# Kernel optimization log

Measured on AMD Instinct MI355X. Metric: run time of the kernel, lower is better.

## Reference

```python
import jax, jax.numpy as jnp
import numpy as np

EPS = 1e-6


def _rmsnorm(x, w, eps=EPS):
    # x: (..., d); normalize over last dim
    ms = jnp.mean(jnp.square(x), axis=-1, keepdims=True)
    return x * jax.lax.rsqrt(ms + eps) * w


def setup_inputs() -> dict:
    key = jax.random.key(0)
    ks = jax.random.split(key, 5)
    B, S, D = 2, 2048, 2048
    n_heads, n_kv = 16, 4
    d_head = D // n_heads  # 128
    sd = 1.0 / np.sqrt(D)
    return {
        "x": jax.random.normal(ks[0], (B, S, D), dtype=jnp.float32),
        "wq": jax.random.normal(ks[1], (D, n_heads * d_head), dtype=jnp.float32) * sd,
        "wk": jax.random.normal(ks[2], (D, n_kv * d_head), dtype=jnp.float32) * sd,
        "wv": jax.random.normal(ks[3], (D, n_kv * d_head), dtype=jnp.float32) * sd,
        "wo": jax.random.normal(ks[4], (D, D), dtype=jnp.float32) * sd,
        "q_norm_w": jnp.ones((d_head,), dtype=jnp.float32),
        "k_norm_w": jnp.ones((d_head,), dtype=jnp.float32),
    }


def reference(x, wq, wk, wv, wo, q_norm_w, k_norm_w):
    B, S, D = x.shape
    n_heads, n_kv = 16, 4
    groups = n_heads // n_kv
    d_head = D // n_heads

    # QKV projections (bias=False)
    q = (x @ wq).reshape(B, S, n_kv, groups, d_head)  # q heads grouped by kv head
    k = (x @ wk).reshape(B, S, n_kv, d_head)
    v = (x @ wv).reshape(B, S, n_kv, d_head)

    # qk RMSNorm over d_head
    q = _rmsnorm(q, q_norm_w)
    k = _rmsnorm(k, k_norm_w)

    # GQA attention without materializing expanded K/V:
    # scores: (B, n_kv, groups, S_q, S_k)
    scale = 1.0 / jnp.sqrt(jnp.asarray(d_head, dtype=x.dtype))
    scores = jnp.einsum('bskgd,btkd->bkgst', q, k) * scale
    causal = jnp.tril(jnp.ones((S, S), dtype=bool))
    scores = jnp.where(causal, scores, jnp.asarray(-jnp.inf, dtype=scores.dtype))
    attn = jax.nn.softmax(scores, axis=-1)
    out = jnp.einsum('bkgst,btkd->bskgd', attn, v)  # (B, S, n_kv, groups, d_head)
    out = out.reshape(B, S, D)
    return out @ wo
```

## Files before the change

kernel.cpp:

```cpp
#include <hip/hip_runtime.h>
#include <hip/hip_bf16.h>
#include <stdint.h>

typedef unsigned short u16;
typedef __attribute__((ext_vector_type(8))) short short8;
typedef __attribute__((ext_vector_type(4))) float f32x4;
typedef __attribute__((ext_vector_type(16))) float f32x16;

__device__ __forceinline__ u16 f2bf(float f){
  union { __hip_bfloat16 h; u16 u; } v; v.h = __float2bfloat16(f); return v.u;
}
__device__ __forceinline__ float bf2f(u16 h){
  union { uint32_t u; float f; } v; v.u = ((uint32_t)h) << 16;
  return v.f;
}
__device__ __forceinline__ f32x4 mfma16(short8 a, short8 b, f32x4 c){
  return __builtin_amdgcn_mfma_f32_16x16x32_bf16(a, b, c, 0, 0, 0);
}
__device__ __forceinline__ f32x16 mfma32(short8 a, short8 b, f32x16 c){
  return __builtin_amdgcn_mfma_f32_32x32x16_bf16(a, b, c, 0, 0, 0);
}
__device__ __forceinline__ void gl_lds16(const u16* g, u16* l){
  __builtin_amdgcn_global_load_lds((const __attribute__((address_space(1))) void*)g,
                                   (__attribute__((address_space(3))) void*)l, 16, 0, 0);
}
template<int N> __device__ __forceinline__ void waitvm(){
  if constexpr (N==0) asm volatile("s_waitcnt vmcnt(0)" ::: "memory");
  else if constexpr (N==2) asm volatile("s_waitcnt vmcnt(2)" ::: "memory");
  else if constexpr (N==4) asm volatile("s_waitcnt vmcnt(4)" ::: "memory");
  else if constexpr (N==8) asm volatile("s_waitcnt vmcnt(8)" ::: "memory");
  else static_assert(N==0 || N==2 || N==4 || N==8, "unsupported vmcnt");
}
__device__ __forceinline__ void phase_sep(){
  __builtin_amdgcn_sched_barrier(0);
  __builtin_amdgcn_s_barrier();
  __builtin_amdgcn_sched_barrier(0);
}
__device__ __forceinline__ uint32_t cvtpk(float lo, float hi){
  uint32_t r;
  asm("v_cvt_pk_bf16_f32 %0, %1, %2" : "=v"(r) : "v"(lo), "v"(hi));
  return r;
}

__global__ __launch_bounds__(256) void cvt_x(const float* __restrict__ s,
                                             u16* __restrict__ d, int n4){
  const int i = blockIdx.x*256 + threadIdx.x;
  if (i >= n4) return;
  const float4 v = ((const float4*)s)[i];
  ushort4 pk;
  pk.x = f2bf(v.x); pk.y = f2bf(v.y); pk.z = f2bf(v.z); pk.w = f2bf(v.w);
  ((ushort4*)d)[i] = pk;
}

__global__ __launch_bounds__(256) void transpose_cvt(const float* __restrict__ src,
    u16* __restrict__ dst, int R, int C)
{
  __shared__ float tile[32][33];
  const int tx = threadIdx.x, ty = threadIdx.y;
  const int c0 = blockIdx.x << 5, r0 = blockIdx.y << 5;
  #pragma unroll
  for (int i=0;i<4;i++)
    tile[ty + (i<<3)][tx] = src[(size_t)(r0 + ty + (i<<3))*C + c0 + tx];
  __syncthreads();
  #pragma unroll
  for (int i=0;i<4;i++)
    dst[(size_t)(c0 + ty + (i<<3))*R + r0 + tx] = f2bf(tile[tx][ty + (i<<3)]);
}

__global__ __launch_bounds__(256) void v_transpose(const u16* __restrict__ qkv,
    u16* __restrict__ vT)
{
  __shared__ u16 tile[32][33];
  const int tx = threadIdx.x, ty = threadIdx.y;
  const int s0 = blockIdx.x << 5, d0 = blockIdx.y << 5;
  const int bk = blockIdx.z; const int b = bk >> 2, kv = bk & 3;
  const u16* src = qkv + (size_t)b*2048*3072 + 2560 + kv*128;
  #pragma unroll
  for (int i=0;i<4;i++)
    tile[ty + (i<<3)][tx] = src[(size_t)(s0 + ty + (i<<3))*3072 + d0 + tx];
  __syncthreads();
  u16* dst = vT + (size_t)((b<<2)+kv)*128*2048;
  #pragma unroll
  for (int i=0;i<4;i++)
    dst[(size_t)(d0 + ty + (i<<3))*2048 + s0 + tx] = tile[tx][ty + (i<<3)];
}

__global__ __launch_bounds__(256) void rmsnorm_qk(u16* __restrict__ qkv,
    const float* __restrict__ qw, const float* __restrict__ kw)
{
  const int lane = threadIdx.x & 63;
  const int rid = blockIdx.x*4 + (threadIdx.x >> 6);
  const int row = rid / 20;
  const int slot = rid % 20;
  u16* p = qkv + (size_t)row*3072 + slot*128 + (lane<<1);
  const u16 r0 = p[0], r1 = p[1];
  const float a = bf2f(r0), c = bf2f(r1);
  float ss = a*a + c*c;
  #pragma unroll
  for (int off=1; off<64; off<<=1) ss += __shfl_xor(ss, off);
  float sc = rsqrtf(ss*(1.0f/128.0f) + 1e-6f);
  if (slot < 16) sc *= 0.1275187952317199f;
  const float* wp = (slot < 16) ? qw : kw;
  const float w0 = wp[lane<<1], w1 = wp[(lane<<1)+1];
  p[0] = f2bf(a*sc*w0);
  p[1] = f2bf(c*sc*w1);
}

template<int BM, int CBF16>
__global__ __launch_bounds__(512, 2) void gemm8(const u16* __restrict__ A,
    const u16* __restrict__ BT, void* __restrict__ Cp,
    int M, int N, int K, int ldc)
{
  constexpr int MF   = BM/32;
  constexpr int MQ   = MF/2;
  constexpr int AH   = BM/2;
  constexpr int ASZ  = AH*64;
  constexpr int DBUF = 2*ASZ + 16384;
  constexpr int WV   = (BM==256) ? 4 : 2;
  __shared__ u16 lds[2*DBUF];
  const int tid = threadIdx.x;
  const int w = tid >> 6, lane = tid & 63;
  const int l15 = lane & 15, lg = lane >> 4;
  const int wm = w >> 2, wn = w & 3;
  const int nbx = N >> 8;
  const int nwg = gridDim.x;
  int bid = blockIdx.x;
  bid = (bid & 7) * (nwg >> 3) + (bid >> 3);
  const int m0 = (bid / nbx) * BM;
  const int n0 = (bid % nbx) << 8;

  const u16* gA0 = A  + (size_t)m0*K;
  const u16* gA1 = gA0 + (size_t)AH*K;
  const u16* gB0 = BT + (size_t)n0*K;
  const u16* gB1 = gB0 + (size_t)128*K;

  auto slotA = [&](int d, int h)->u16*{ return lds + d*DBUF + h*ASZ; };
  auto slotB = [&](int d, int h)->u16*{ return lds + d*DBUF + 2*ASZ + h*8192; };

  auto stage_half = [&](const u16* gbase, int kt, u16* sbase, int rows){
    const int iters = rows >> 6;
    for (int i=0;i<iters;i++){
      const int p = (i<<9) + tid;
      const int row = p>>3, sg = (p&7) ^ (row&7);
      gl_lds16(gbase + (size_t)row*K + (kt<<6) + (sg<<3), sbase + (p<<3));
    }
  };
  auto stA = [&](int kt, int d){ stage_half(gA0, kt, slotA(d,0), AH);
                                 stage_half(gA1, kt, slotA(d,1), AH); };
  auto stB = [&](int kt, int d){ stage_half(gB0, kt, slotB(d,0), 128);
                                 stage_half(gB1, kt, slotB(d,1), 128); };
  auto frag_at = [&](const u16* buf, int lrow, int kk)->short8{
    const int s = ((kk<<2)+lg) ^ (lrow&7);
    return *(const short8*)(buf + (((lrow<<3)+s)<<3));
  };

  short8 af[MQ][2], bfe[2][2], bfo[2][2];
  f32x4 acc[MF][4];
  #pragma unroll
  for (int m=0;m<MF;m++)
    #pragma unroll
    for (int n=0;n<4;n++) acc[m][n] = (f32x4){0.f,0.f,0.f,0.f};

  const int bh = wn>>1;
  const int brow0 = ((wn&1)<<6) + l15;

  auto rd_a = [&](const u16* buf, int mq){
    #pragma unroll
    for (int m=0;m<MQ;m++)
      #pragma unroll
      for (int kk=0;kk<2;kk++)
        af[m][kk] = frag_at(buf, mq*(BM>>2) + (m<<4) + l15, kk);
  };
  auto rd_b = [&](const u16* buf, int nq, short8 (*dst)[2]){
    #pragma unroll
    for (int n=0;n<2;n++)
      #pragma unroll
      for (int kk=0;kk<2;kk++)
        dst[n][kk] = frag_at(buf, brow0 + (nq<<5) + (n<<4), kk);
  };
  auto do_mfma = [&](int mb, int nb, short8 (*bf)[2]){
    __builtin_amdgcn_s_setprio(1);
    #pragma unroll
    for (int m=0;m<MQ;m++)
      #pragma unroll
      for (int n=0;n<2;n++)
        #pragma unroll
        for (int kk=0;kk<2;kk++)
          acc[mb+m][nb+n] = mfma16(af[m][kk], bf[n][kk], acc[mb+m][nb+n]);
    __builtin_amdgcn_s_setprio(0);
  };

  stA(0,0); stB(0,0); stA(1,1);
  waitvm<WV>();
  phase_sep();

  const int niter = K >> 7;
  for (int i=0; i<niter; ++i){
    const bool full = (i+1 < niter);
    const int t1 = 2*i+1;
    rd_a(slotA(0,wm), 0); rd_b(slotB(0,bh), 0, bfe);
    stB(t1, 1);
    phase_sep();
    do_mfma(0, 0, bfe);
    phase_sep();
    rd_b(slotB(0,bh), 1, bfo);
    phase_sep();
    do_mfma(0, 2, bfo);
    phase_sep();
    rd_a(slotA(0,wm), 1);
    phase_sep();
    do_mfma(MQ, 2, bfo);
    phase_sep();
    rd_b(slotB(0,bh), 0, bfe);
    if (full) stA(t1+1, 0);
    phase_sep();
    do_mfma(MQ, 0, bfe);
    if (full) waitvm<WV>(); else waitvm<0>();
    phase_sep();
    rd_a(slotA(1,wm), 0); rd_b(slotB(1,bh), 0, bfe);
    if (full) stB(t1+1, 0);
    phase_sep();
    do_mfma(0, 0, bfe);
    phase_sep();
    rd_b(slotB(1,bh), 1, bfo);
    phase_sep();
    do_mfma(0, 2, bfo);
    phase_sep();
    rd_a(slotA(1,wm), 1);
    phase_sep();
    do_mfma(MQ, 2, bfo);
    phase_sep();
    rd_b(slotB(1,bh), 0, bfe);
    if (full) stA(t1+2, 1);
    phase_sep();
    do_mfma(MQ, 0, bfe);
    if (full) waitvm<WV>();
    phase_sep();
  }

  #pragma unroll
  for (int m=0;m<MF;m++){
    #pragma unroll
    for (int n=0;n<4;n++){
      const int col = n0 + (wn<<6) + (n<<4) + l15;
      #pragma unroll
      for (int r=0;r<4;r++){
        const int row = m0 + wm*AH + (m<<4) + (lg<<2) + r;
        if (CBF16) ((u16*)Cp)[(size_t)row*ldc + col] = f2bf(acc[m][n][r]);
        else       ((float*)Cp)[(size_t)row*ldc + col] = acc[m][n][r];
      }
    }
  }
}

__global__ __launch_bounds__(256, 2) void attn_kernel(const u16* __restrict__ qkv,
    const u16* __restrict__ vT, u16* __restrict__ aout)
{
  __shared__ u16 Klds[2][8192];
  __shared__ u16 Vlds[8192];
  const int tid = threadIdx.x;
  const int w = tid >> 6, lane = tid & 63;
  const int l31 = lane & 31, hi = lane >> 5;
  const int bx = blockIdx.x, h = blockIdx.y, b = blockIdx.z;
  const int qI = b ? bx : (15 - bx);
  const int kvh = h >> 2;
  const int qb = qI*128 + (w<<5);
  const int nt = 2*qI + 2;

  const u16* qkvb = qkv + (size_t)b*2048*3072;
  short8 qf[8];
  {
    const u16* qp = qkvb + (size_t)(qb + l31)*3072 + h*128 + hi*8;
    #pragma unroll
    for (int kk=0;kk<8;kk++) qf[kk] = *(const short8*)(qp + kk*16);
  }
  f32x16 oacc[4];
  #pragma unroll
  for (int d=0;d<4;d++)
    #pragma unroll
    for (int r=0;r<16;r++) oacc[d][r] = 0.f;
  float m_run = -__builtin_inff(), lsum = 0.f;

  const u16* kb_ = qkvb + 2048 + kvh*128;
  const u16* vb_ = vT + (size_t)((b<<2)+kvh)*128*2048;

  auto stageK = [&](int t, int buf){
    #pragma unroll
    for (int i=0;i<4;i++){
      const int u = (i<<8) + tid;
      const int row = u>>4, d0 = (u&15) ^ (row&15);
      gl_lds16(kb_ + (size_t)((t<<6)+row)*3072 + (d0<<3), &Klds[buf][u<<3]);
    }
  };
  auto stageV = [&](int t){
    #pragma unroll
    for (int i=0;i<4;i++){
      const int u = (i<<8) + tid;
      const int rp = u>>4, z = (u&15) ^ (rp&15);
      const int d = (rp<<1) + (z>>3), k8 = z&7;
      gl_lds16(vb_ + (size_t)d*2048 + (t<<6) + (k8<<3), &Vlds[u<<3]);
    }
  };

  stageK(0, 0);
  int kbuf = 0;
  for (int t=0; t<nt; ++t){
    const bool pre = (t+1 < nt);
    stageV(t);
    if (pre) stageK(t+1, kbuf^1);
    if (pre) waitvm<8>(); else waitvm<4>();
    phase_sep();
    const int t0 = t<<6;
    const bool act = (t0 <= qb + 31);
    uint32_t paw[4][4];
    if (act){
      f32x16 s0, s1;
      #pragma unroll
      for (int r=0;r<16;r++){ s0[r] = 0.f; s1[r] = 0.f; }
      #pragma unroll
      for (int kk=0;kk<8;kk++){
        const int d0 = (kk<<1) + hi;
        const short8 k0 = *(const short8*)&Klds[kbuf][((l31<<4) + (d0 ^ (l31&15)))<<3];
        s0 = mfma32(k0, qf[kk], s0);
        const int r1 = 32 + l31;
        const short8 k1 = *(const short8*)&Klds[kbuf][((r1<<4) + (d0 ^ (r1&15)))<<3];
        s1 = mfma32(k1, qf[kk], s1);
      }
      if (t0 + 63 > qb){
        const int qrel = qb + l31 - t0;
        #pragma unroll
        for (int r=0;r<16;r++){
          const int kloc = (r&3) + ((r>>2)<<3) + (hi<<2);
          if (kloc      > qrel) s0[r] = -__builtin_inff();
          if (kloc + 32 > qrel) s1[r] = -__builtin_inff();
        }
      }
      float t8[8];
      #pragma unroll
      for (int i=0;i<8;i++) t8[i] = fmaxf(fmaxf(s0[i], s0[i+8]), fmaxf(s1[i], s1[i+8]));
      #pragma unroll
      for (int i=0;i<4;i++) t8[i] = fmaxf(t8[i], t8[i+4]);
      float mx = fmaxf(fmaxf(t8[0],t8[1]), fmaxf(t8[2],t8[3]));
      mx = fmaxf(mx, __shfl_xor(mx, 32));
      const bool noskip = !__all(mx - m_run <= 8.0f);
      const float mnew = noskip ? fmaxf(m_run, mx) : m_run;
      float rs = 0.f;
      #pragma unroll
      for (int i=0;i<16;i++){
        s0[i] = __builtin_amdgcn_exp2f(s0[i] - mnew);
        s1[i] = __builtin_amdgcn_exp2f(s1[i] - mnew);
        rs += s0[i] + s1[i];
      }
      rs += __shfl_xor(rs, 32);
      if (noskip){
        const float corr = __builtin_amdgcn_exp2f(m_run - mnew);
        m_run = mnew;
        lsum = lsum*corr + rs;
        #pragma unroll
        for (int r=0;r<16;r++){
          const float cr = __shfl(corr, (r&3) + ((r>>2)<<3) + (hi<<2));
          #pragma unroll
          for (int db=0;db<4;db++) oacc[db][r] *= cr;
        }
      } else {
        lsum += rs;
      }
      #pragma unroll
      for (int kk=0;kk<4;kk++){
        const int base = (kk&1)<<3;
        float v0,v1,v2,v3,v4,v5,v6,v7;
        if (kk<2){ v0=s0[base+0]; v1=s0[base+1]; v2=s0[base+2]; v3=s0[base+3];
                   v4=s0[base+4]; v5=s0[base+5]; v6=s0[base+6]; v7=s0[base+7]; }
        else     { v0=s1[base+0]; v1=s1[base+1]; v2=s1[base+2]; v3=s1[base+3];
                   v4=s1[base+4]; v5=s1[base+5]; v6=s1[base+6]; v7=s1[base+7]; }
        uint32_t a0 = cvtpk(v0, v1), a1 = cvtpk(v2, v3);
        uint32_t b0 = cvtpk(v4, v5), b1 = cvtpk(v6, v7);
        asm volatile("v_permlane32_swap_b32 %0, %1" : "+v"(a0), "+v"(b0));
        asm volatile("v_permlane32_swap_b32 %0, %1" : "+v"(a1), "+v"(b1));
        paw[kk][0] = a0; paw[kk][1] = a1; paw[kk][2] = b0; paw[kk][3] = b1;
      }
    }
    if (pre) waitvm<4>(); else waitvm<0>();
    phase_sep();
    if (act){
      #pragma unroll
      for (int kk=0;kk<4;kk++){
        union { uint32_t w[4]; short8 v; } pu;
        pu.w[0]=paw[kk][0]; pu.w[1]=paw[kk][1]; pu.w[2]=paw[kk][2]; pu.w[3]=paw[kk][3];
        const short8 pa = pu.v;
        #pragma unroll
        for (int db=0;db<4;db++){
          const int d = (db<<5) + l31, rp = d>>1;
          const int sl = (((d&1)<<3) | ((kk<<1)+hi)) ^ (rp&15);
          const short8 vv = *(const short8*)&Vlds[((rp<<4)+sl)<<3];
          oacc[db] = mfma32(pa, vv, oacc[db]);
        }
      }
    }
    phase_sep();
    kbuf ^= 1;
  }

  const float inv = 1.0f / lsum;
  #pragma unroll
  for (int r=0;r<16;r++){
    const int qr = (r&3) + ((r>>2)<<3) + (hi<<2);
    const float ivr = __shfl(inv, qr);
    u16* op = aout + (size_t)(b*2048 + qb + qr)*2048 + h*128 + l31;
    #pragma unroll
    for (int db=0;db<4;db++)
      op[db<<5] = f2bf(oacc[db][r] * ivr);
  }
}

extern "C" void kernel_launch(void* const* d_in, const int* in_sizes, int n_in,
                              void* d_out, int out_size, void* d_ws, size_t ws_size,
                              hipStream_t stream) {
  const float* x  = (const float*)d_in[0];
  const float* wq = (const float*)d_in[1];
  const float* wk = (const float*)d_in[2];
  const float* wv = (const float*)d_in[3];
  const float* wo = (const float*)d_in[4];
  const float* qw = (const float*)d_in[5];
  const float* kw = (const float*)d_in[6];
  char* ws = (char*)d_ws;
  u16* xbf   = (u16*)(ws);
  u16* wqkvT = (u16*)(ws + 16777216);
  u16* woT   = (u16*)(ws + 29360128);
  u16* qkv   = (u16*)(ws + 37748736);
  u16* vT    = (u16*)(ws + 62914560);
  float* out = (float*)d_out;

  dim3 tb(32,8);
  cvt_x<<<8192, 256, 0, stream>>>(x, xbf, 2097152);
  transpose_cvt<<<dim3(64,64), tb, 0, stream>>>(wq, wqkvT,             2048, 2048);
  transpose_cvt<<<dim3(16,64), tb, 0, stream>>>(wk, wqkvT + 2048*2048, 2048, 512);
  transpose_cvt<<<dim3(16,64), tb, 0, stream>>>(wv, wqkvT + 2560*2048, 2048, 512);
  transpose_cvt<<<dim3(64,64), tb, 0, stream>>>(wo, woT,               2048, 2048);
  gemm8<256,1><<<192, 512, 0, stream>>>(xbf, wqkvT, qkv, 4096, 3072, 2048, 3072);
  rmsnorm_qk<<<20480, 256, 0, stream>>>(qkv, qw, kw);
  v_transpose<<<dim3(64,4,8), tb, 0, stream>>>(qkv, vT);
  attn_kernel<<<dim3(16,16,2), 256, 0, stream>>>(qkv, vT, xbf);
  gemm8<128,0><<<256, 512, 0, stream>>>(xbf, woT, out, 4096, 2048, 2048, 2048);
}
```

Baseline: 196.6 us.

## Split long causal attention rows across two blocks and merge with a combine kernel

Query blocks 8-15 now have their KV range split into two halves, each handled by a separate workgroup that writes unnormalized partial outputs plus running max and sum. A new combine kernel merges the two halves with log-sum-exp weights. A constant table orders the 768 work items longest-first for load balancing, and launch bounds go up to 3 blocks per CU. The aim is to fix the causal load imbalance and tail effect, at the cost of an extra kernel launch and fp32 partial traffic. The partials are staged in the output buffer and the weight workspace before those are overwritten.

```diff
diff --git a/kernel.cpp b/kernel.cpp
--- a/kernel.cpp
+++ b/kernel.cpp
@@ -6,6 +6,10 @@
 typedef __attribute__((ext_vector_type(8))) short short8;
 typedef __attribute__((ext_vector_type(4))) float f32x4;
 typedef __attribute__((ext_vector_type(16))) float f32x16;
+
+__constant__ unsigned char TJ[24] = {
+  39, 15, 31, 14, 30, 38, 13, 29, 12, 28, 37, 11,
+  27, 10, 26, 36,  9, 25,  8, 24, 35, 34, 33, 32 };
 
 __device__ __forceinline__ u16 f2bf(float f){
   union { __hip_bfloat16 h; u16 u; } v; v.h = __float2bfloat16(f); return v.u;
@@ -253,19 +257,25 @@
   }
 }
 
-__global__ __launch_bounds__(256, 2) void attn_kernel(const u16* __restrict__ qkv,
-    const u16* __restrict__ vT, u16* __restrict__ aout)
+__global__ __launch_bounds__(256, 3) void attn_kernel(const u16* __restrict__ qkv,
+    const u16* __restrict__ vT, u16* __restrict__ aout,
+    float* __restrict__ partial, float2* __restrict__ mlbuf)
 {
   __shared__ u16 Klds[2][8192];
   __shared__ u16 Vlds[8192];
   const int tid = threadIdx.x;
   const int w = tid >> 6, lane = tid & 63;
   const int l31 = lane & 31, hi = lane >> 5;
-  const int bx = blockIdx.x, h = blockIdx.y, b = blockIdx.z;
-  const int qI = b ? bx : (15 - bx);
-  const int kvh = h >> 2;
+  const int bid = blockIdx.x;
+  const int j = bid >> 5;
+  const int grp = bid & 31;
+  const int b = grp >> 4, kvh = (grp >> 2) & 3, hh = grp & 3;
+  const int h = (kvh<<2) + hh;
+  const unsigned v_ = TJ[j];
+  const int qI = v_ & 15, s = v_ >> 4;
+  const int tb = (s == 1) ? (qI + 1) : 0;
+  const int te = (s == 0) ? (qI + 1) : (2*qI + 2);
   const int qb = qI*128 + (w<<5);
-  const int nt = 2*qI + 2;
 
   const u16* qkvb = qkv + (size_t)b*2048*3072;
   short8 qf[8];
@@ -302,114 +312,152 @@
     }
   };
 
-  stageK(0, 0);
+  stageK(tb, 0);
   int kbuf = 0;
-  for (int t=0; t<nt; ++t){
-    const bool pre = (t+1 < nt);
+  for (int t=tb; t<te; ++t){
+    const bool pre = (t+1 < te);
     stageV(t);
     if (pre) stageK(t+1, kbuf^1);
     if (pre) waitvm<8>(); else waitvm<4>();
     phase_sep();
     const int t0 = t<<6;
-    const bool act = (t0 <= qb + 31);
+    f32x16 s0, s1;
+    #pragma unroll
+    for (int r=0;r<16;r++){ s0[r] = 0.f; s1[r] = 0.f; }
+    #pragma unroll
+    for (int kk=0;kk<8;kk++){
+      const int d0 = (kk<<1) + hi;
+      const short8 k0 = *(const short8*)&Klds[kbuf][((l31<<4) + (d0 ^ (l31&15)))<<3];
+      s0 = mfma32(k0, qf[kk], s0);
+      const int r1 = 32 + l31;
+      const short8 k1 = *(const short8*)&Klds[kbuf][((r1<<4) + (d0 ^ (r1&15)))<<3];
+      s1 = mfma32(k1, qf[kk], s1);
+    }
+    if (t0 + 63 > qb){
+      const int qrel = qb + l31 - t0;
+      #pragma unroll
+      for (int r=0;r<16;r++){
+        const int kloc = (r&3) + ((r>>2)<<3) + (hi<<2);
+        if (kloc      > qrel) s0[r] = -__builtin_inff();
+        if (kloc + 32 > qrel) s1[r] = -__builtin_inff();
+      }
+    }
+    float t8[8];
+    #pragma unroll
+    for (int i=0;i<8;i++) t8[i] = fmaxf(fmaxf(s0[i], s0[i+8]), fmaxf(s1[i], s1[i+8]));
+    #pragma unroll
+    for (int i=0;i<4;i++) t8[i] = fmaxf(t8[i], t8[i+4]);
+    float mx = fmaxf(fmaxf(t8[0],t8[1]), fmaxf(t8[2],t8[3]));
+    mx = fmaxf(mx, __shfl_xor(mx, 32));
+    const bool noskip = !__all(mx - m_run <= 8.0f);
+    const float mnew = noskip ? fmaxf(m_run, mx) : m_run;
+    float rs = 0.f;
+    #pragma unroll
+    for (int i=0;i<16;i++){
+      s0[i] = __builtin_amdgcn_exp2f(s0[i] - mnew);
+      s1[i] = __builtin_amdgcn_exp2f(s1[i] - mnew);
+      rs += s0[i] + s1[i];
+    }
+    rs += __shfl_xor(rs, 32);
+    if (noskip){
+      const float corr = __builtin_amdgcn_exp2f(m_run - mnew);
+      m_run = mnew;
+      lsum = lsum*corr + rs;
+      #pragma unroll
+      for (int r=0;r<16;r++){
+        const float cr = __shfl(corr, (r&3) + ((r>>2)<<3) + (hi<<2));
+        #pragma unroll
+        for (int db=0;db<4;db++) oacc[db][r] *= cr;
+      }
+    } else {
+      lsum += rs;
+    }
     uint32_t paw[4][4];
-    if (act){
-      f32x16 s0, s1;
-      #pragma unroll
-      for (int r=0;r<16;r++){ s0[r] = 0.f; s1[r] = 0.f; }
-      #pragma unroll
-      for (int kk=0;kk<8;kk++){
-        const int d0 = (kk<<1) + hi;
-        const short8 k0 = *(const short8*)&Klds[kbuf][((l31<<4) + (d0 ^ (l31&15)))<<3];
-        s0 = mfma32(k0, qf[kk], s0);
-        const int r1 = 32 + l31;
-        const short8 k1 = *(const short8*)&Klds[kbuf][((r1<<4) + (d0 ^ (r1&15)))<<3];
-        s1 = mfma32(k1, qf[kk], s1);
+    #pragma unroll
+    for (int kk=0;kk<4;kk++){
+      const int base = (kk&1)<<3;
+      float v0,v1,v2,v3,v4,v5,v6,v7;
+      if (kk<2){ v0=s0[base+0]; v1=s0[base+1]; v2=s0[base+2]; v3=s0[base+3];
+                 v4=s0[base+4]; v5=s0[base+5]; v6=s0[base+6]; v7=s0[base+7]; }
+      else     { v0=s1[base+0]; v1=s1[base+1]; v2=s1[base+2]; v3=s1[base+3];
+                 v4=s1[base+4]; v5=s1[base+5]; v6=s1[base+6]; v7=s1[base+7]; }
+      uint32_t a0 = cvtpk(v0, v1), a1 = cvtpk(v2, v3);
+      uint32_t b0 = cvtpk(v4, v5), b1 = cvtpk(v6, v7);
+      asm volatile("v_permlane32_swap_b32 %0, %1" : "+v"(a0), "+v"(b0));
+      asm volatile("v_permlane32_swap_b32 %0, %1" : "+v"(a1), "+v"(b1));
+      paw[kk][0] = a0; paw[kk][1] = a1; paw[kk][2] = b0; paw[kk][3] = b1;
+    }
+    if (pre) waitvm<4>(); else waitvm<0>();
+    phase_sep();
+    #pragma unroll
+    for (int kk=0;kk<4;kk++){
+      union { uint32_t w[4]; short8 v; } pu;
+      pu.w[0]=paw[kk][0]; pu.w[1]=paw[kk][1]; pu.w[2]=paw[kk][2]; pu.w[3]=paw[kk][3];
+      const short8 pa = pu.v;
+      #pragma unroll
+      for (int db=0;db<4;db++){
+        const int d = (db<<5) + l31, rp = d>>1;
+        const int sl = (((d&1)<<3) | ((kk<<1)+hi)) ^ (rp&15);
+        const short8 vv = *(const short8*)&Vlds[((rp<<4)+sl)<<3];
+        oacc[db] = mfma32(pa, vv, oacc[db]);
       }
-      if (t0 + 63 > qb){
-        const int qrel = qb + l31 - t0;
-        #pragma unroll
-        for (int r=0;r<16;r++){
-          const int kloc = (r&3) + ((r>>2)<<3) + (hi<<2);
-          if (kloc      > qrel) s0[r] = -__builtin_inff();
-          if (kloc + 32 > qrel) s1[r] = -__builtin_inff();
-        }
-      }
-      float t8[8];
-      #pragma unroll
-      for (int i=0;i<8;i++) t8[i] = fmaxf(fmaxf(s0[i], s0[i+8]), fmaxf(s1[i], s1[i+8]));
-      #pragma unroll
-      for (int i=0;i<4;i++) t8[i] = fmaxf(t8[i], t8[i+4]);
-      float mx = fmaxf(fmaxf(t8[0],t8[1]), fmaxf(t8[2],t8[3]));
-      mx = fmaxf(mx, __shfl_xor(mx, 32));
-      const bool noskip = !__all(mx - m_run <= 8.0f);
-      const float mnew = noskip ? fmaxf(m_run, mx) : m_run;
-      float rs = 0.f;
-      #pragma unroll
-      for (int i=0;i<16;i++){
-        s0[i] = __builtin_amdgcn_exp2f(s0[i] - mnew);
-        s1[i] = __builtin_amdgcn_exp2f(s1[i] - mnew);
-        rs += s0[i] + s1[i];
-      }
-      rs += __shfl_xor(rs, 32);
-      if (noskip){
-        const float corr = __builtin_amdgcn_exp2f(m_run - mnew);
-        m_run = mnew;
-        lsum = lsum*corr + rs;
-        #pragma unroll
-        for (int r=0;r<16;r++){
-          const float cr = __shfl(corr, (r&3) + ((r>>2)<<3) + (hi<<2));
-          #pragma unroll
-          for (int db=0;db<4;db++) oacc[db][r] *= cr;
-        }
-      } else {
-        lsum += rs;
-      }
-      #pragma unroll
-      for (int kk=0;kk<4;kk++){
-        const int base = (kk&1)<<3;
-        float v0,v1,v2,v3,v4,v5,v6,v7;
-        if (kk<2){ v0=s0[base+0]; v1=s0[base+1]; v2=s0[base+2]; v3=s0[base+3];
-                   v4=s0[base+4]; v5=s0[base+5]; v6=s0[base+6]; v7=s0[base+7]; }
-        else     { v0=s1[base+0]; v1=s1[base+1]; v2=s1[base+2]; v3=s1[base+3];
-                   v4=s1[base+4]; v5=s1[base+5]; v6=s1[base+6]; v7=s1[base+7]; }
-        uint32_t a0 = cvtpk(v0, v1), a1 = cvtpk(v2, v3);
-        uint32_t b0 = cvtpk(v4, v5), b1 = cvtpk(v6, v7);
-        asm volatile("v_permlane32_swap_b32 %0, %1" : "+v"(a0), "+v"(b0));
-        asm volatile("v_permlane32_swap_b32 %0, %1" : "+v"(a1), "+v"(b1));
-        paw[kk][0] = a0; paw[kk][1] = a1; paw[kk][2] = b0; paw[kk][3] = b1;
-      }
-    }
-    if (pre) waitvm<4>(); else waitvm<0>();
-    phase_sep();
-    if (act){
-      #pragma unroll
-      for (int kk=0;kk<4;kk++){
-        union { uint32_t w[4]; short8 v; } pu;
-        pu.w[0]=paw[kk][0]; pu.w[1]=paw[kk][1]; pu.w[2]=paw[kk][2]; pu.w[3]=paw[kk][3];
-        const short8 pa = pu.v;
-        #pragma unroll
-        for (int db=0;db<4;db++){
-          const int d = (db<<5) + l31, rp = d>>1;
-          const int sl = (((d&1)<<3) | ((kk<<1)+hi)) ^ (rp&15);
-          const short8 vv = *(const short8*)&Vlds[((rp<<4)+sl)<<3];
-          oacc[db] = mfma32(pa, vv, oacc[db]);
-        }
-      }
     }
     phase_sep();
     kbuf ^= 1;
   }
 
-  const float inv = 1.0f / lsum;
-  #pragma unroll
-  for (int r=0;r<16;r++){
-    const int qr = (r&3) + ((r>>2)<<3) + (hi<<2);
-    const float ivr = __shfl(inv, qr);
-    u16* op = aout + (size_t)(b*2048 + qb + qr)*2048 + h*128 + l31;
-    #pragma unroll
-    for (int db=0;db<4;db++)
-      op[db<<5] = f2bf(oacc[db][r] * ivr);
+  if (s == 2){
+    const float inv = 1.0f / lsum;
+    #pragma unroll
+    for (int r=0;r<16;r++){
+      const int qr = (r&3) + ((r>>2)<<3) + (hi<<2);
+      const float ivr = __shfl(inv, qr);
+      u16* op = aout + (size_t)(b*2048 + qI*128 + (w<<5) + qr)*2048 + h*128 + l31;
+      #pragma unroll
+      for (int db=0;db<4;db++)
+        op[db<<5] = f2bf(oacc[db][r] * ivr);
+    }
+  } else {
+    const int tau = (((b<<4) + h)<<3) + (qI - 8);
+    float* pO = partial + (size_t)((tau<<1)+s)*16384;
+    #pragma unroll
+    for (int r=0;r<16;r++){
+      const int qr = (r&3) + ((r>>2)<<3) + (hi<<2);
+      float* pr = pO + ((w<<5)+qr)*128 + l31;
+      #pragma unroll
+      for (int db=0;db<4;db++) pr[db<<5] = oacc[db][r];
+    }
+    if (hi == 0)
+      mlbuf[((tau<<1)+s)*128 + (w<<5) + l31] = make_float2(m_run, lsum);
+  }
+}
+
+__global__ __launch_bounds__(256) void attn_combine(const float* __restrict__ partial,
+    const float2* __restrict__ mlbuf, u16* __restrict__ aout)
+{
+  const int tau = blockIdx.x;
+  const int b = tau >> 7, h = (tau >> 3) & 15, qI = (tau & 7) + 8;
+  const int row = threadIdx.x >> 1;
+  const int c0 = (threadIdx.x & 1) << 6;
+  const float2 ml0 = mlbuf[(tau<<1)*128 + row];
+  const float2 ml1 = mlbuf[((tau<<1)+1)*128 + row];
+  const float M = fmaxf(ml0.x, ml1.x);
+  float w0 = __builtin_amdgcn_exp2f(ml0.x - M);
+  float w1 = __builtin_amdgcn_exp2f(ml1.x - M);
+  const float inv = 1.0f / (w0*ml0.y + w1*ml1.y);
+  w0 *= inv; w1 *= inv;
+  const float4* P0 = (const float4*)(partial + (size_t)(tau<<1)*16384 + row*128 + c0);
+  const float4* P1 = (const float4*)(partial + (size_t)((tau<<1)+1)*16384 + row*128 + c0);
+  ushort4* op = (ushort4*)(aout + (size_t)(b*2048 + qI*128 + row)*2048 + h*128 + c0);
+  #pragma unroll
+  for (int i=0;i<16;i++){
+    const float4 a = P0[i], c = P1[i];
+    ushort4 o;
+    o.x = f2bf(w0*a.x + w1*c.x);
+    o.y = f2bf(w0*a.y + w1*c.y);
+    o.z = f2bf(w0*a.z + w1*c.z);
+    o.w = f2bf(w0*a.w + w1*c.w);
+    op[i] = o;
   }
 }
 
@@ -429,6 +477,7 @@
   u16* woT   = (u16*)(ws + 29360128);
   u16* qkv   = (u16*)(ws + 37748736);
   u16* vT    = (u16*)(ws + 62914560);
+  float2* ml = (float2*)(ws + 16777216);
   float* out = (float*)d_out;
 
   dim3 tb(32,8);
@@ -440,6 +489,7 @@
   gemm8<256,1><<<192, 512, 0, stream>>>(xbf, wqkvT, qkv, 4096, 3072, 2048, 3072);
   rmsnorm_qk<<<20480, 256, 0, stream>>>(qkv, qw, kw);
   v_transpose<<<dim3(64,4,8), tb, 0, stream>>>(qkv, vT);
-  attn_kernel<<<dim3(16,16,2), 256, 0, stream>>>(qkv, vT, xbf);
+  attn_kernel<<<768, 256, 0, stream>>>(qkv, vT, xbf, out, ml);
+  attn_combine<<<256, 256, 0, stream>>>(out, ml, xbf);
   gemm8<128,0><<<256, 512, 0, stream>>>(xbf, woT, out, 4096, 2048, 2048, 2048);
 }
```

New measurement: 234.4 us. 1.19x slower.

## Pair high and low causal query tiles per block sharing K/V tiles

Applied to the files above, without the earlier changes.

Each attention block now handles two 128-row query tiles, one from the top and one from the bottom of the causal range, so every block does equal work and each K/V tile staged in LDS serves both. V is double-buffered alongside K, with loads issued two tiles ahead, and the grid is halved with launch bounds lowered to one block per SIMD slot. This aims to remove causal load imbalance and halve K/V traffic per query row. In exchange, register pressure roughly doubles (two accumulator sets), occupancy drops, and only 256 blocks are launched.

```diff
diff --git a/kernel.cpp b/kernel.cpp
--- a/kernel.cpp
+++ b/kernel.cpp
@@ -253,163 +253,189 @@
   }
 }
 
-__global__ __launch_bounds__(256, 2) void attn_kernel(const u16* __restrict__ qkv,
+__global__ __launch_bounds__(256, 1) void attn_kernel(const u16* __restrict__ qkv,
     const u16* __restrict__ vT, u16* __restrict__ aout)
 {
   __shared__ u16 Klds[2][8192];
-  __shared__ u16 Vlds[8192];
+  __shared__ u16 Vlds[2][8192];
   const int tid = threadIdx.x;
   const int w = tid >> 6, lane = tid & 63;
   const int l31 = lane & 31, hi = lane >> 5;
-  const int bx = blockIdx.x, h = blockIdx.y, b = blockIdx.z;
-  const int qI = b ? bx : (15 - bx);
+  const int h = blockIdx.x, p = blockIdx.y, b = blockIdx.z;
   const int kvh = h >> 2;
-  const int qb = qI*128 + (w<<5);
-  const int nt = 2*qI + 2;
+  const int hq0 = (15-p) << 7, lq0 = p << 7;
+  const int nt = 32 - 2*p;
+  const int qbH = hq0 + (w<<5), qbL = lq0 + (w<<5);
 
   const u16* qkvb = qkv + (size_t)b*2048*3072;
-  short8 qf[8];
+  short8 qfH[8], qfL[8];
   {
-    const u16* qp = qkvb + (size_t)(qb + l31)*3072 + h*128 + hi*8;
-    #pragma unroll
-    for (int kk=0;kk<8;kk++) qf[kk] = *(const short8*)(qp + kk*16);
+    const u16* qpH = qkvb + (size_t)(qbH + l31)*3072 + h*128 + hi*8;
+    const u16* qpL = qkvb + (size_t)(qbL + l31)*3072 + h*128 + hi*8;
+    #pragma unroll
+    for (int kk=0;kk<8;kk++){ qfH[kk] = *(const short8*)(qpH + kk*16);
+                              qfL[kk] = *(const short8*)(qpL + kk*16); }
   }
-  f32x16 oacc[4];
+  f32x16 oaccH[4], oaccL[4];
   #pragma unroll
   for (int d=0;d<4;d++)
     #pragma unroll
-    for (int r=0;r<16;r++) oacc[d][r] = 0.f;
-  float m_run = -__builtin_inff(), lsum = 0.f;
+    for (int r=0;r<16;r++){ oaccH[d][r] = 0.f; oaccL[d][r] = 0.f; }
+  float mH = -__builtin_inff(), lH = 0.f;
+  float mL = -__builtin_inff(), lL = 0.f;
 
   const u16* kb_ = qkvb + 2048 + kvh*128;
   const u16* vb_ = vT + (size_t)((b<<2)+kvh)*128*2048;
 
-  auto stageK = [&](int t, int buf){
+  auto stageKV = [&](int t, int buf){
     #pragma unroll
     for (int i=0;i<4;i++){
       const int u = (i<<8) + tid;
       const int row = u>>4, d0 = (u&15) ^ (row&15);
       gl_lds16(kb_ + (size_t)((t<<6)+row)*3072 + (d0<<3), &Klds[buf][u<<3]);
     }
-  };
-  auto stageV = [&](int t){
     #pragma unroll
     for (int i=0;i<4;i++){
       const int u = (i<<8) + tid;
       const int rp = u>>4, z = (u&15) ^ (rp&15);
       const int d = (rp<<1) + (z>>3), k8 = z&7;
-      gl_lds16(vb_ + (size_t)d*2048 + (t<<6) + (k8<<3), &Vlds[u<<3]);
-    }
-  };
-
-  stageK(0, 0);
-  int kbuf = 0;
+      gl_lds16(vb_ + (size_t)d*2048 + (t<<6) + (k8<<3), &Vlds[buf][u<<3]);
+    }
+  };
+
+  auto qksm = [&](const u16* Kb, const short8* qf, f32x16* oacc,
+                  float& m_run, float& lsum, int qb, int t0,
+                  uint32_t paw[4][4]){
+    f32x16 s0, s1;
+    #pragma unroll
+    for (int r=0;r<16;r++){ s0[r] = 0.f; s1[r] = 0.f; }
+    #pragma unroll
+    for (int kk=0;kk<8;kk++){
+      const int d0 = (kk<<1) + hi;
+      const short8 k0 = *(const short8*)&Kb[((l31<<4) + (d0 ^ (l31&15)))<<3];
+      s0 = mfma32(k0, qf[kk], s0);
+      const int r1 = 32 + l31;
+      const short8 k1 = *(const short8*)&Kb[((r1<<4) + (d0 ^ (r1&15)))<<3];
+      s1 = mfma32(k1, qf[kk], s1);
+    }
+    if (t0 + 63 > qb){
+      const int qrel = qb + l31 - t0;
+      #pragma unroll
+      for (int r=0;r<16;r++){
+        const int kloc = (r&3) + ((r>>2)<<3) + (hi<<2);
+        if (kloc      > qrel) s0[r] = -__builtin_inff();
+        if (kloc + 32 > qrel) s1[r] = -__builtin_inff();
+      }
+    }
+    float t8[8];
+    #pragma unroll
+    for (int i=0;i<8;i++) t8[i] = fmaxf(fmaxf(s0[i], s0[i+8]), fmaxf(s1[i], s1[i+8]));
+    #pragma unroll
+    for (int i=0;i<4;i++) t8[i] = fmaxf(t8[i], t8[i+4]);
+    float mx = fmaxf(fmaxf(t8[0],t8[1]), fmaxf(t8[2],t8[3]));
+    mx = fmaxf(mx, __shfl_xor(mx, 32));
+    const bool noskip = !__all(mx - m_run <= 8.0f);
+    const float mnew = noskip ? fmaxf(m_run, mx) : m_run;
+    float rs = 0.f;
+    #pragma unroll
+    for (int i=0;i<16;i++){
+      s0[i] = __builtin_amdgcn_exp2f(s0[i] - mnew);
+      s1[i] = __builtin_amdgcn_exp2f(s1[i] - mnew);
+      rs += s0[i] + s1[i];
+    }
+    rs += __shfl_xor(rs, 32);
+    if (noskip){
+      const float corr = __builtin_amdgcn_exp2f(m_run - mnew);
+      m_run = mnew;
+      lsum = lsum*corr + rs;
+      #pragma unroll
+      for (int r=0;r<16;r++){
+        const float cr = __shfl(corr, (r&3) + ((r>>2)<<3) + (hi<<2));
+        #pragma unroll
+        for (int db=0;db<4;db++) oacc[db][r] *= cr;
+      }
+    } else {
+      lsum += rs;
+    }
+    #pragma unroll
+    for (int kk=0;kk<4;kk++){
+      const int base = (kk&1)<<3;
+      float v0,v1,v2,v3,v4,v5,v6,v7;
+      if (kk<2){ v0=s0[base+0]; v1=s0[base+1]; v2=s0[base+2]; v3=s0[base+3];
+                 v4=s0[base+4]; v5=s0[base+5]; v6=s0[base+6]; v7=s0[base+7]; }
+      else     { v0=s1[base+0]; v1=s1[base+1]; v2=s1[base+2]; v3=s1[base+3];
+                 v4=s1[base+4]; v5=s1[base+5]; v6=s1[base+6]; v7=s1[base+7]; }
+      uint32_t a0 = cvtpk(v0, v1), a1 = cvtpk(v2, v3);
+      uint32_t b0 = cvtpk(v4, v5), b1 = cvtpk(v6, v7);
+      asm volatile("v_permlane32_swap_b32 %0, %1" : "+v"(a0), "+v"(b0));
+      asm volatile("v_permlane32_swap_b32 %0, %1" : "+v"(a1), "+v"(b1));
+      paw[kk][0] = a0; paw[kk][1] = a1; paw[kk][2] = b0; paw[kk][3] = b1;
+    }
+  };
+
+  auto mkpa = [&](const uint32_t pw[4])->short8{
+    union { uint32_t w[4]; short8 v; } pu;
+    pu.w[0]=pw[0]; pu.w[1]=pw[1]; pu.w[2]=pw[2]; pu.w[3]=pw[3];
+    return pu.v;
+  };
+
+  stageKV(0, 0);
+  if (nt > 1) stageKV(1, 1);
   for (int t=0; t<nt; ++t){
-    const bool pre = (t+1 < nt);
-    stageV(t);
-    if (pre) stageK(t+1, kbuf^1);
-    if (pre) waitvm<8>(); else waitvm<4>();
+    const int kbuf = t & 1;
+    if (t+1 < nt) waitvm<8>(); else waitvm<0>();
     phase_sep();
     const int t0 = t<<6;
-    const bool act = (t0 <= qb + 31);
-    uint32_t paw[4][4];
-    if (act){
-      f32x16 s0, s1;
-      #pragma unroll
-      for (int r=0;r<16;r++){ s0[r] = 0.f; s1[r] = 0.f; }
-      #pragma unroll
-      for (int kk=0;kk<8;kk++){
-        const int d0 = (kk<<1) + hi;
-        const short8 k0 = *(const short8*)&Klds[kbuf][((l31<<4) + (d0 ^ (l31&15)))<<3];
-        s0 = mfma32(k0, qf[kk], s0);
-        const int r1 = 32 + l31;
-        const short8 k1 = *(const short8*)&Klds[kbuf][((r1<<4) + (d0 ^ (r1&15)))<<3];
-        s1 = mfma32(k1, qf[kk], s1);
-      }
-      if (t0 + 63 > qb){
-        const int qrel = qb + l31 - t0;
-        #pragma unroll
-        for (int r=0;r<16;r++){
-          const int kloc = (r&3) + ((r>>2)<<3) + (hi<<2);
-          if (kloc      > qrel) s0[r] = -__builtin_inff();
-          if (kloc + 32 > qrel) s1[r] = -__builtin_inff();
-        }
-      }
-      float t8[8];
-      #pragma unroll
-      for (int i=0;i<8;i++) t8[i] = fmaxf(fmaxf(s0[i], s0[i+8]), fmaxf(s1[i], s1[i+8]));
-      #pragma unroll
-      for (int i=0;i<4;i++) t8[i] = fmaxf(t8[i], t8[i+4]);
-      float mx = fmaxf(fmaxf(t8[0],t8[1]), fmaxf(t8[2],t8[3]));
-      mx = fmaxf(mx, __shfl_xor(mx, 32));
-      const bool noskip = !__all(mx - m_run <= 8.0f);
-      const float mnew = noskip ? fmaxf(m_run, mx) : m_run;
-      float rs = 0.f;
-      #pragma unroll
-      for (int i=0;i<16;i++){
-        s0[i] = __builtin_amdgcn_exp2f(s0[i] - mnew);
-        s1[i] = __builtin_amdgcn_exp2f(s1[i] - mnew);
-        rs += s0[i] + s1[i];
-      }
-      rs += __shfl_xor(rs, 32);
-      if (noskip){
-        const float corr = __builtin_amdgcn_exp2f(m_run - mnew);
-        m_run = mnew;
-        lsum = lsum*corr + rs;
-        #pragma unroll
-        for (int r=0;r<16;r++){
-          const float cr = __shfl(corr, (r&3) + ((r>>2)<<3) + (hi<<2));
-          #pragma unroll
-          for (int db=0;db<4;db++) oacc[db][r] *= cr;
-        }
-      } else {
-        lsum += rs;
-      }
+    const bool actH = t0 <= qbH + 31;
+    const bool actL = t0 <= qbL + 31;
+    uint32_t pawH[4][4], pawL[4][4];
+    if (actH) qksm(&Klds[kbuf][0], qfH, oaccH, mH, lH, qbH, t0, pawH);
+    if (actL) qksm(&Klds[kbuf][0], qfL, oaccL, mL, lL, qbL, t0, pawL);
+    if (actL){
       #pragma unroll
       for (int kk=0;kk<4;kk++){
-        const int base = (kk&1)<<3;
-        float v0,v1,v2,v3,v4,v5,v6,v7;
-        if (kk<2){ v0=s0[base+0]; v1=s0[base+1]; v2=s0[base+2]; v3=s0[base+3];
-                   v4=s0[base+4]; v5=s0[base+5]; v6=s0[base+6]; v7=s0[base+7]; }
-        else     { v0=s1[base+0]; v1=s1[base+1]; v2=s1[base+2]; v3=s1[base+3];
-                   v4=s1[base+4]; v5=s1[base+5]; v6=s1[base+6]; v7=s1[base+7]; }
-        uint32_t a0 = cvtpk(v0, v1), a1 = cvtpk(v2, v3);
-        uint32_t b0 = cvtpk(v4, v5), b1 = cvtpk(v6, v7);
-        asm volatile("v_permlane32_swap_b32 %0, %1" : "+v"(a0), "+v"(b0));
-        asm volatile("v_permlane32_swap_b32 %0, %1" : "+v"(a1), "+v"(b1));
-        paw[kk][0] = a0; paw[kk][1] = a1; paw[kk][2] = b0; paw[kk][3] = b1;
-      }
-    }
-    if (pre) waitvm<4>(); else waitvm<0>();
-    phase_sep();
-    if (act){
-      #pragma unroll
-      for (int kk=0;kk<4;kk++){
-        union { uint32_t w[4]; short8 v; } pu;
-        pu.w[0]=paw[kk][0]; pu.w[1]=paw[kk][1]; pu.w[2]=paw[kk][2]; pu.w[3]=paw[kk][3];
-        const short8 pa = pu.v;
+        const short8 paH = mkpa(pawH[kk]);
+        const short8 paL = mkpa(pawL[kk]);
         #pragma unroll
         for (int db=0;db<4;db++){
           const int d = (db<<5) + l31, rp = d>>1;
           const int sl = (((d&1)<<3) | ((kk<<1)+hi)) ^ (rp&15);
-          const short8 vv = *(const short8*)&Vlds[((rp<<4)+sl)<<3];
-          oacc[db] = mfma32(pa, vv, oacc[db]);
+          const short8 vv = *(const short8*)&Vlds[kbuf][((rp<<4)+sl)<<3];
+          oaccH[db] = mfma32(paH, vv, oaccH[db]);
+          oaccL[db] = mfma32(paL, vv, oaccL[db]);
         }
       }
-    }
-    phase_sep();
-    kbuf ^= 1;
+    } else if (actH){
+      #pragma unroll
+      for (int kk=0;kk<4;kk++){
+        const short8 paH = mkpa(pawH[kk]);
+        #pragma unroll
+        for (int db=0;db<4;db++){
+          const int d = (db<<5) + l31, rp = d>>1;
+          const int sl = (((d&1)<<3) | ((kk<<1)+hi)) ^ (rp&15);
+          const short8 vv = *(const short8*)&Vlds[kbuf][((rp<<4)+sl)<<3];
+          oaccH[db] = mfma32(paH, vv, oaccH[db]);
+        }
+      }
+    }
+    phase_sep();
+    if (t+2 < nt) stageKV(t+2, kbuf);
   }
 
-  const float inv = 1.0f / lsum;
+  const float invH = 1.0f / lH;
+  const float invL = 1.0f / lL;
   #pragma unroll
   for (int r=0;r<16;r++){
     const int qr = (r&3) + ((r>>2)<<3) + (hi<<2);
-    const float ivr = __shfl(inv, qr);
-    u16* op = aout + (size_t)(b*2048 + qb + qr)*2048 + h*128 + l31;
-    #pragma unroll
-    for (int db=0;db<4;db++)
-      op[db<<5] = f2bf(oacc[db][r] * ivr);
+    const float ivH = __shfl(invH, qr);
+    const float ivL = __shfl(invL, qr);
+    u16* opH = aout + (size_t)(b*2048 + qbH + qr)*2048 + h*128 + l31;
+    u16* opL = aout + (size_t)(b*2048 + qbL + qr)*2048 + h*128 + l31;
+    #pragma unroll
+    for (int db=0;db<4;db++){
+      opH[db<<5] = f2bf(oaccH[db][r] * ivH);
+      opL[db<<5] = f2bf(oaccL[db][r] * ivL);
+    }
   }
 }
 
@@ -440,6 +466,6 @@
   gemm8<256,1><<<192, 512, 0, stream>>>(xbf, wqkvT, qkv, 4096, 3072, 2048, 3072);
   rmsnorm_qk<<<20480, 256, 0, stream>>>(qkv, qw, kw);
   v_transpose<<<dim3(64,4,8), tb, 0, stream>>>(qkv, vT);
-  attn_kernel<<<dim3(16,16,2), 256, 0, stream>>>(qkv, vT, xbf);
+  attn_kernel<<<dim3(16,8,2), 256, 0, stream>>>(qkv, vT, xbf);
   gemm8<128,0><<<256, 512, 0, stream>>>(xbf, woT, out, 4096, 2048, 2048, 2048);
 }
```

Result: slower. 212.3 us (+8.0%).

## Merge prep kernels, fuse Q RMSNorm into attention, drop act guard

Applied to the files above, without the earlier changes.

Replaces the x conversion and four weight-transpose launches with a single prep kernel that dispatches on block index. Q RMSNorm moves into the attention kernel's Q-fragment load, so the separate norm kernel only touches K, which shrinks it five-fold and avoids a round trip of Q through memory. The per-tile 'act' guard is removed from the attention loop because every wave's tiles are active under the causal tile count. The costs are extra per-element work at attention start and a weight read from global memory for each Q element.

```diff
diff --git a/kernel.cpp b/kernel.cpp
--- a/kernel.cpp
+++ b/kernel.cpp
@@ -42,22 +42,31 @@
   return r;
 }
 
-__global__ __launch_bounds__(256) void cvt_x(const float* __restrict__ s,
-                                             u16* __restrict__ d, int n4){
-  const int i = blockIdx.x*256 + threadIdx.x;
-  if (i >= n4) return;
-  const float4 v = ((const float4*)s)[i];
-  ushort4 pk;
-  pk.x = f2bf(v.x); pk.y = f2bf(v.y); pk.z = f2bf(v.z); pk.w = f2bf(v.w);
-  ((ushort4*)d)[i] = pk;
-}
-
-__global__ __launch_bounds__(256) void transpose_cvt(const float* __restrict__ src,
-    u16* __restrict__ dst, int R, int C)
+__global__ __launch_bounds__(256) void prep(const float* __restrict__ x,
+    const float* __restrict__ wq, const float* __restrict__ wk,
+    const float* __restrict__ wv, const float* __restrict__ wo,
+    u16* __restrict__ xbf, u16* __restrict__ wqkvT, u16* __restrict__ woT)
 {
   __shared__ float tile[32][33];
-  const int tx = threadIdx.x, ty = threadIdx.y;
-  const int c0 = blockIdx.x << 5, r0 = blockIdx.y << 5;
+  int bid = blockIdx.x;
+  const int tid = threadIdx.x;
+  if (bid < 8192){
+    const int i = bid*256 + tid;
+    const float4 v = ((const float4*)x)[i];
+    ushort4 pk;
+    pk.x = f2bf(v.x); pk.y = f2bf(v.y); pk.z = f2bf(v.z); pk.w = f2bf(v.w);
+    ((ushort4*)xbf)[i] = pk;
+    return;
+  }
+  bid -= 8192;
+  const float* src; u16* dst; int C, bx, by;
+  if (bid < 4096){ src = wq; dst = wqkvT; C = 2048; bx = bid & 63; by = bid >> 6; }
+  else if (bid < 8192){ bid -= 4096; src = wo; dst = woT; C = 2048; bx = bid & 63; by = bid >> 6; }
+  else if (bid < 9216){ bid -= 8192; src = wk; dst = wqkvT + 2048*2048; C = 512; bx = bid & 15; by = bid >> 4; }
+  else { bid -= 9216; src = wv; dst = wqkvT + 2560*2048; C = 512; bx = bid & 15; by = bid >> 4; }
+  const int R = 2048;
+  const int tx = tid & 31, ty = tid >> 5;
+  const int c0 = bx << 5, r0 = by << 5;
   #pragma unroll
   for (int i=0;i<4;i++)
     tile[ty + (i<<3)][tx] = src[(size_t)(r0 + ty + (i<<3))*C + c0 + tx];
@@ -85,23 +94,21 @@
     dst[(size_t)(d0 + ty + (i<<3))*2048 + s0 + tx] = tile[tx][ty + (i<<3)];
 }
 
-__global__ __launch_bounds__(256) void rmsnorm_qk(u16* __restrict__ qkv,
-    const float* __restrict__ qw, const float* __restrict__ kw)
+__global__ __launch_bounds__(256) void rmsnorm_k(u16* __restrict__ qkv,
+    const float* __restrict__ kw)
 {
   const int lane = threadIdx.x & 63;
   const int rid = blockIdx.x*4 + (threadIdx.x >> 6);
-  const int row = rid / 20;
-  const int slot = rid % 20;
-  u16* p = qkv + (size_t)row*3072 + slot*128 + (lane<<1);
+  const int row = rid >> 2;
+  const int slot = rid & 3;
+  u16* p = qkv + (size_t)row*3072 + 2048 + slot*128 + (lane<<1);
   const u16 r0 = p[0], r1 = p[1];
   const float a = bf2f(r0), c = bf2f(r1);
   float ss = a*a + c*c;
   #pragma unroll
   for (int off=1; off<64; off<<=1) ss += __shfl_xor(ss, off);
-  float sc = rsqrtf(ss*(1.0f/128.0f) + 1e-6f);
-  if (slot < 16) sc *= 0.1275187952317199f;
-  const float* wp = (slot < 16) ? qw : kw;
-  const float w0 = wp[lane<<1], w1 = wp[(lane<<1)+1];
+  const float sc = rsqrtf(ss*(1.0f/128.0f) + 1e-6f);
+  const float w0 = kw[lane<<1], w1 = kw[(lane<<1)+1];
   p[0] = f2bf(a*sc*w0);
   p[1] = f2bf(c*sc*w1);
 }
@@ -254,7 +261,8 @@
 }
 
 __global__ __launch_bounds__(256, 2) void attn_kernel(const u16* __restrict__ qkv,
-    const u16* __restrict__ vT, u16* __restrict__ aout)
+    const u16* __restrict__ vT, const float* __restrict__ qw,
+    u16* __restrict__ aout)
 {
   __shared__ u16 Klds[2][8192];
   __shared__ u16 Vlds[8192];
@@ -273,6 +281,24 @@
     const u16* qp = qkvb + (size_t)(qb + l31)*3072 + h*128 + hi*8;
     #pragma unroll
     for (int kk=0;kk<8;kk++) qf[kk] = *(const short8*)(qp + kk*16);
+    float ss = 0.f;
+    #pragma unroll
+    for (int kk=0;kk<8;kk++)
+      #pragma unroll
+      for (int e=0;e<8;e++){
+        const float v = bf2f((u16)qf[kk][e]);
+        ss += v*v;
+      }
+    ss += __shfl_xor(ss, 32);
+    const float sc = rsqrtf(ss*(1.0f/128.0f) + 1e-6f) * 0.1275187952317199f;
+    #pragma unroll
+    for (int kk=0;kk<8;kk++){
+      #pragma unroll
+      for (int e=0;e<8;e++){
+        const float wv_ = qw[kk*16 + hi*8 + e];
+        qf[kk][e] = (short)f2bf(bf2f((u16)qf[kk][e]) * sc * wv_);
+      }
+    }
   }
   f32x16 oacc[4];
   #pragma unroll
@@ -311,90 +337,85 @@
     if (pre) waitvm<8>(); else waitvm<4>();
     phase_sep();
     const int t0 = t<<6;
-    const bool act = (t0 <= qb + 31);
+    f32x16 s0, s1;
+    #pragma unroll
+    for (int r=0;r<16;r++){ s0[r] = 0.f; s1[r] = 0.f; }
+    #pragma unroll
+    for (int kk=0;kk<8;kk++){
+      const int d0 = (kk<<1) + hi;
+      const short8 k0 = *(const short8*)&Klds[kbuf][((l31<<4) + (d0 ^ (l31&15)))<<3];
+      s0 = mfma32(k0, qf[kk], s0);
+      const int r1 = 32 + l31;
+      const short8 k1 = *(const short8*)&Klds[kbuf][((r1<<4) + (d0 ^ (r1&15)))<<3];
+      s1 = mfma32(k1, qf[kk], s1);
+    }
+    if (t0 + 63 > qb){
+      const int qrel = qb + l31 - t0;
+      #pragma unroll
+      for (int r=0;r<16;r++){
+        const int kloc = (r&3) + ((r>>2)<<3) + (hi<<2);
+        if (kloc      > qrel) s0[r] = -__builtin_inff();
+        if (kloc + 32 > qrel) s1[r] = -__builtin_inff();
+      }
+    }
+    float t8[8];
+    #pragma unroll
+    for (int i=0;i<8;i++) t8[i] = fmaxf(fmaxf(s0[i], s0[i+8]), fmaxf(s1[i], s1[i+8]));
+    #pragma unroll
+    for (int i=0;i<4;i++) t8[i] = fmaxf(t8[i], t8[i+4]);
+    float mx = fmaxf(fmaxf(t8[0],t8[1]), fmaxf(t8[2],t8[3]));
+    mx = fmaxf(mx, __shfl_xor(mx, 32));
+    const bool noskip = !__all(mx - m_run <= 8.0f);
+    const float mnew = noskip ? fmaxf(m_run, mx) : m_run;
+    float rs = 0.f;
+    #pragma unroll
+    for (int i=0;i<16;i++){
+      s0[i] = __builtin_amdgcn_exp2f(s0[i] - mnew);
+      s1[i] = __builtin_amdgcn_exp2f(s1[i] - mnew);
+      rs += s0[i] + s1[i];
+    }
+    rs += __shfl_xor(rs, 32);
+    if (noskip){
+      const float corr = __builtin_amdgcn_exp2f(m_run - mnew);
+      m_run = mnew;
+      lsum = lsum*corr + rs;
+      #pragma unroll
+      for (int r=0;r<16;r++){
+        const float cr = __shfl(corr, (r&3) + ((r>>2)<<3) + (hi<<2));
+        #pragma unroll
+        for (int db=0;db<4;db++) oacc[db][r] *= cr;
+      }
+    } else {
+      lsum += rs;
+    }
     uint32_t paw[4][4];
-    if (act){
-      f32x16 s0, s1;
-      #pragma unroll
-      for (int r=0;r<16;r++){ s0[r] = 0.f; s1[r] = 0.f; }
-      #pragma unroll
-      for (int kk=0;kk<8;kk++){
-        const int d0 = (kk<<1) + hi;
-        const short8 k0 = *(const short8*)&Klds[kbuf][((l31<<4) + (d0 ^ (l31&15)))<<3];
-        s0 = mfma32(k0, qf[kk], s0);
-        const int r1 = 32 + l31;
-        const short8 k1 = *(const short8*)&Klds[kbuf][((r1<<4) + (d0 ^ (r1&15)))<<3];
-        s1 = mfma32(k1, qf[kk], s1);
-      }
-      if (t0 + 63 > qb){
-        const int qrel = qb + l31 - t0;
-        #pragma unroll
-        for (int r=0;r<16;r++){
-          const int kloc = (r&3) + ((r>>2)<<3) + (hi<<2);
-          if (kloc      > qrel) s0[r] = -__builtin_inff();
-          if (kloc + 32 > qrel) s1[r] = -__builtin_inff();
-        }
-      }
-      float t8[8];
-      #pragma unroll
-      for (int i=0;i<8;i++) t8[i] = fmaxf(fmaxf(s0[i], s0[i+8]), fmaxf(s1[i], s1[i+8]));
-      #pragma unroll
-      for (int i=0;i<4;i++) t8[i] = fmaxf(t8[i], t8[i+4]);
-      float mx = fmaxf(fmaxf(t8[0],t8[1]), fmaxf(t8[2],t8[3]));
-      mx = fmaxf(mx, __shfl_xor(mx, 32));
-      const bool noskip = !__all(mx - m_run <= 8.0f);
-      const float mnew = noskip ? fmaxf(m_run, mx) : m_run;
-      float rs = 0.f;
-      #pragma unroll
-      for (int i=0;i<16;i++){
-        s0[i] = __builtin_amdgcn_exp2f(s0[i] - mnew);
-        s1[i] = __builtin_amdgcn_exp2f(s1[i] - mnew);
-        rs += s0[i] + s1[i];
-      }
-      rs += __shfl_xor(rs, 32);
-      if (noskip){
-        const float corr = __builtin_amdgcn_exp2f(m_run - mnew);
-        m_run = mnew;
-        lsum = lsum*corr + rs;
-        #pragma unroll
-        for (int r=0;r<16;r++){
-          const float cr = __shfl(corr, (r&3) + ((r>>2)<<3) + (hi<<2));
-          #pragma unroll
-          for (int db=0;db<4;db++) oacc[db][r] *= cr;
-        }
-      } else {
-        lsum += rs;
-      }
-      #pragma unroll
-      for (int kk=0;kk<4;kk++){
-        const int base = (kk&1)<<3;
-        float v0,v1,v2,v3,v4,v5,v6,v7;
-        if (kk<2){ v0=s0[base+0]; v1=s0[base+1]; v2=s0[base+2]; v3=s0[base+3];
-                   v4=s0[base+4]; v5=s0[base+5]; v6=s0[base+6]; v7=s0[base+7]; }
-        else     { v0=s1[base+0]; v1=s1[base+1]; v2=s1[base+2]; v3=s1[base+3];
-                   v4=s1[base+4]; v5=s1[base+5]; v6=s1[base+6]; v7=s1[base+7]; }
-        uint32_t a0 = cvtpk(v0, v1), a1 = cvtpk(v2, v3);
-        uint32_t b0 = cvtpk(v4, v5), b1 = cvtpk(v6, v7);
-        asm volatile("v_permlane32_swap_b32 %0, %1" : "+v"(a0), "+v"(b0));
-        asm volatile("v_permlane32_swap_b32 %0, %1" : "+v"(a1), "+v"(b1));
-        paw[kk][0] = a0; paw[kk][1] = a1; paw[kk][2] = b0; paw[kk][3] = b1;
-      }
+    #pragma unroll
+    for (int kk=0;kk<4;kk++){
+      const int base = (kk&1)<<3;
+      float v0,v1,v2,v3,v4,v5,v6,v7;
+      if (kk<2){ v0=s0[base+0]; v1=s0[base+1]; v2=s0[base+2]; v3=s0[base+3];
+                 v4=s0[base+4]; v5=s0[base+5]; v6=s0[base+6]; v7=s0[base+7]; }
+      else     { v0=s1[base+0]; v1=s1[base+1]; v2=s1[base+2]; v3=s1[base+3];
+                 v4=s1[base+4]; v5=s1[base+5]; v6=s1[base+6]; v7=s1[base+7]; }
+      uint32_t a0 = cvtpk(v0, v1), a1 = cvtpk(v2, v3);
+      uint32_t b0 = cvtpk(v4, v5), b1 = cvtpk(v6, v7);
+      asm volatile("v_permlane32_swap_b32 %0, %1" : "+v"(a0), "+v"(b0));
+      asm volatile("v_permlane32_swap_b32 %0, %1" : "+v"(a1), "+v"(b1));
+      paw[kk][0] = a0; paw[kk][1] = a1; paw[kk][2] = b0; paw[kk][3] = b1;
     }
     if (pre) waitvm<4>(); else waitvm<0>();
     phase_sep();
-    if (act){
-      #pragma unroll
-      for (int kk=0;kk<4;kk++){
-        union { uint32_t w[4]; short8 v; } pu;
-        pu.w[0]=paw[kk][0]; pu.w[1]=paw[kk][1]; pu.w[2]=paw[kk][2]; pu.w[3]=paw[kk][3];
-        const short8 pa = pu.v;
-        #pragma unroll
-        for (int db=0;db<4;db++){
-          const int d = (db<<5) + l31, rp = d>>1;
-          const int sl = (((d&1)<<3) | ((kk<<1)+hi)) ^ (rp&15);
-          const short8 vv = *(const short8*)&Vlds[((rp<<4)+sl)<<3];
-          oacc[db] = mfma32(pa, vv, oacc[db]);
-        }
+    #pragma unroll
+    for (int kk=0;kk<4;kk++){
+      union { uint32_t w[4]; short8 v; } pu;
+      pu.w[0]=paw[kk][0]; pu.w[1]=paw[kk][1]; pu.w[2]=paw[kk][2]; pu.w[3]=paw[kk][3];
+      const short8 pa = pu.v;
+      #pragma unroll
+      for (int db=0;db<4;db++){
+        const int d = (db<<5) + l31, rp = d>>1;
+        const int sl = (((d&1)<<3) | ((kk<<1)+hi)) ^ (rp&15);
+        const short8 vv = *(const short8*)&Vlds[((rp<<4)+sl)<<3];
+        oacc[db] = mfma32(pa, vv, oacc[db]);
       }
     }
     phase_sep();
@@ -431,15 +452,10 @@
   u16* vT    = (u16*)(ws + 62914560);
   float* out = (float*)d_out;
 
-  dim3 tb(32,8);
-  cvt_x<<<8192, 256, 0, stream>>>(x, xbf, 2097152);
-  transpose_cvt<<<dim3(64,64), tb, 0, stream>>>(wq, wqkvT,             2048, 2048);
-  transpose_cvt<<<dim3(16,64), tb, 0, stream>>>(wk, wqkvT + 2048*2048, 2048, 512);
-  transpose_cvt<<<dim3(16,64), tb, 0, stream>>>(wv, wqkvT + 2560*2048, 2048, 512);
-  transpose_cvt<<<dim3(64,64), tb, 0, stream>>>(wo, woT,               2048, 2048);
+  prep<<<18432, 256, 0, stream>>>(x, wq, wk, wv, wo, xbf, wqkvT, woT);
   gemm8<256,1><<<192, 512, 0, stream>>>(xbf, wqkvT, qkv, 4096, 3072, 2048, 3072);
-  rmsnorm_qk<<<20480, 256, 0, stream>>>(qkv, qw, kw);
-  v_transpose<<<dim3(64,4,8), tb, 0, stream>>>(qkv, vT);
-  attn_kernel<<<dim3(16,16,2), 256, 0, stream>>>(qkv, vT, xbf);
+  rmsnorm_k<<<4096, 256, 0, stream>>>(qkv, kw);
+  v_transpose<<<dim3(64,4,8), dim3(32,8), 0, stream>>>(qkv, vT);
+  attn_kernel<<<dim3(16,16,2), 256, 0, stream>>>(qkv, vT, qw, xbf);
   gemm8<128,0><<<256, 512, 0, stream>>>(xbf, woT, out, 4096, 2048, 2048, 2048);
 }
```

Result: faster. 180.3 us (-8.3%).
